# Performance work log

Hardware: AMD Instinct MI355X
Metric: run time of the kernel (lower is better)

## Reference

```python
import jax, jax.numpy as jnp
import numpy as np

B, T, C, H = 8, 2048, 1024, 64  # batch, time(block_size), n_embd, head_size


def setup_inputs() -> dict:
    key = jax.random.key(0)
    k1, k2, k3, k4 = jax.random.split(key, 4)
    x = jax.random.normal(k1, (B, T, C), dtype=jnp.float32)
    # nn.Linear(n_embd, head_size, bias=False): y = x @ W.T with W [H, C];
    # store as [C, H] so projection is x @ W.
    Wq = jax.random.normal(k2, (C, H), dtype=jnp.float32) * 0.02
    Wk = jax.random.normal(k3, (C, H), dtype=jnp.float32) * 0.02
    Wv = jax.random.normal(k4, (C, H), dtype=jnp.float32) * 0.02
    return {"x": x, "Wq": Wq, "Wk": Wk, "Wv": Wv}


def reference(x, Wq, Wk, Wv):
    # x: [B, T, C]
    Bb, Tt, Cc = x.shape
    q = x @ Wq  # [B, T, H]
    k = x @ Wk  # [B, T, H]
    v = x @ Wv  # [B, T, H]
    # scores = Q @ K^T / sqrt(channels)  -- note: code scales by n_embd, not head_size
    scale = jnp.asarray(Cc, x.dtype) ** 0.5
    scores = jnp.einsum('bth,bsh->bts', q, k) / scale  # [B, T, T]
    # causal mask (decoder=True): lower-triangular allowed
    causal = jnp.tril(jnp.ones((Tt, Tt), dtype=bool))
    scores = jnp.where(causal, scores, -jnp.inf)
    attn = jax.nn.softmax(scores, axis=-1)  # [B, T, T]
    # dropout p=0.0 -> identity
    res = attn @ v  # [B, T, H]
    return res, attn
```

## Files before the change

kernel.cpp:

```cpp
#include <hip/hip_runtime.h>
#include <hip/hip_bf16.h>


typedef __attribute__((ext_vector_type(8))) short bf16x8;
typedef __attribute__((ext_vector_type(4))) float f32x4;

#define NB 8
#define NT 2048
#define NC 1024
#define NH 64

#define VM_DRAIN() asm volatile("s_waitcnt vmcnt(0)" ::: "memory")

__device__ __forceinline__ unsigned short f2bf(float f) {
    unsigned int u = __builtin_bit_cast(unsigned int, f);
    u += 0x7fffu + ((u >> 16) & 1u);
    return (unsigned short)(u >> 16);
}

__device__ __forceinline__ bf16x8 cvt8(float4 a, float4 b) {
    union { bf16x8 v; __hip_bfloat162 h[4]; } u;
    u.h[0] = __float22bfloat162_rn(make_float2(a.x, a.y));
    u.h[1] = __float22bfloat162_rn(make_float2(a.z, a.w));
    u.h[2] = __float22bfloat162_rn(make_float2(b.x, b.y));
    u.h[3] = __float22bfloat162_rn(make_float2(b.z, b.w));
    return u.v;
}

__device__ __forceinline__ void async_ld16(const void* g, const void* l) {
    __builtin_amdgcn_global_load_lds(
        (const __attribute__((address_space(1))) unsigned int*)g,
        (__attribute__((address_space(3))) unsigned int*)(unsigned int)(unsigned long long)l,
        16, 0, 0);
}

__global__ __launch_bounds__(256) void wt_kernel(
        const float* __restrict__ Wq,
        const float* __restrict__ Wk,
        const float* __restrict__ Wv,
        unsigned short* __restrict__ Wt) {
    __shared__ float tile[64][65];
    int m  = blockIdx.x >> 4;
    int k0 = (blockIdx.x & 15) * 64;
    const float* W = (m == 0) ? Wq : ((m == 1) ? Wk : Wv);
    int tid = threadIdx.x;
    for (int i = 0; i < 4; ++i) {
        int f = tid + i * 256;
        int r = f >> 4, c4 = (f & 15) * 4;
        float4 v = *(const float4*)&W[(size_t)(k0 + r) * 64 + c4];
        tile[r][c4 + 0] = v.x; tile[r][c4 + 1] = v.y;
        tile[r][c4 + 2] = v.z; tile[r][c4 + 3] = v.w;
    }
    __syncthreads();
    int n  = tid & 63;
    int kq = (tid >> 6) * 16;
    float scale = (m == 0) ? 0.03125f : 1.0f;
    __attribute__((aligned(16))) unsigned short outv[16];
    for (int j = 0; j < 16; ++j)
        outv[j] = f2bf(tile[kq + j][n] * scale);
    unsigned short* dst = &Wt[(size_t)m * (64 * 1024) + (size_t)n * 1024 + k0 + kq];
    *(uint4*)dst       = *(const uint4*)&outv[0];
    *(uint4*)(dst + 8) = *(const uint4*)&outv[8];
}

__global__ __launch_bounds__(256) void qkv_kernel(
        const float* __restrict__ x,
        const unsigned short* __restrict__ Wt,
        unsigned short* __restrict__ qkv,
        unsigned short* __restrict__ v_t) {
    __shared__ char smem[65536];

    int tid  = threadIdx.x;
    int wave = tid >> 6, lane = tid & 63, quad = lane >> 4, l15 = lane & 15;
    int row0 = blockIdx.x * 32;

    f32x4 acc[2][3];
#pragma unroll
    for (int rt = 0; rt < 2; ++rt)
#pragma unroll
        for (int j = 0; j < 3; ++j) acc[rt][j] = (f32x4){0.f, 0.f, 0.f, 0.f};

#pragma unroll
    for (int i = 0; i < 2; ++i) {
        int s = i * 256 + tid;
        int m = s >> 4, p = s & 15;
        int j = (p & 8) | ((p & 7) ^ (m & 7));
        async_ld16(x + (size_t)(row0 + m) * NC + j * 4,
                   smem + i * 4096 + wave * 1024);
    }
#pragma unroll
    for (int i = 0; i < 6; ++i) {
        int s = i * 256 + tid;
        int n = s >> 3, p = s & 7;
        int j = p ^ (n & 7);
        async_ld16(Wt + (size_t)n * NC + j * 8,
                   smem + 8192 + i * 4096 + wave * 1024);
    }

    int cur = 0;
    for (int kb = 0; kb < 16; ++kb) {
        VM_DRAIN();
        __syncthreads();
        if (kb < 15) {
            char* nb = smem + (cur ^ 1) * 32768;
#pragma unroll
            for (int i = 0; i < 2; ++i) {
                int s = i * 256 + tid;
                int m = s >> 4, p = s & 15;
                int j = (p & 8) | ((p & 7) ^ (m & 7));
                async_ld16(x + (size_t)(row0 + m) * NC + (kb + 1) * 64 + j * 4,
                           nb + i * 4096 + wave * 1024);
            }
#pragma unroll
            for (int i = 0; i < 6; ++i) {
                int s = i * 256 + tid;
                int n = s >> 3, p = s & 7;
                int j = p ^ (n & 7);
                async_ld16(Wt + (size_t)n * NC + (kb + 1) * 64 + j * 8,
                           nb + 8192 + i * 4096 + wave * 1024);
            }
        }
        char* Ab = smem + cur * 32768;
        char* Bb = Ab + 8192;
#pragma unroll
        for (int c = 0; c < 2; ++c) {
            bf16x8 af[2];
#pragma unroll
            for (int rt = 0; rt < 2; ++rt) {
                int m  = rt * 16 + l15;
                int j0 = c * 8 + quad * 2;
                int p0 = (j0 & 8) | ((j0 & 7) ^ (m & 7));
                int p1 = (j0 & 8) | (((j0 + 1) & 7) ^ (m & 7));
                float4 a0 = *(const float4*)(Ab + m * 256 + p0 * 16);
                float4 a1 = *(const float4*)(Ab + m * 256 + p1 * 16);
                af[rt] = cvt8(a0, a1);
            }
#pragma unroll
            for (int jj = 0; jj < 3; ++jj) {
                int n = (wave * 3 + jj) * 16 + l15;
                int p = (c * 4 + quad) ^ (n & 7);
                bf16x8 bf = *(const bf16x8*)(Bb + n * 128 + p * 16);
#pragma unroll
                for (int rt = 0; rt < 2; ++rt)
                    acc[rt][jj] = __builtin_amdgcn_mfma_f32_16x16x32_bf16(
                        af[rt], bf, acc[rt][jj], 0, 0, 0);
            }
        }
        cur ^= 1;
    }

    int b = row0 >> 11;
#pragma unroll
    for (int jj = 0; jj < 3; ++jj) {
        int g   = wave * 3 + jj;
        int mat = g >> 2;
        int col = (g & 3) * 16 + l15;
#pragma unroll
        for (int rt = 0; rt < 2; ++rt) {
            int rowb = row0 + rt * 16 + quad * 4;
            if (mat < 2) {
#pragma unroll
                for (int r = 0; r < 4; ++r)
                    qkv[(size_t)mat * (16384 * 64) + (size_t)(rowb + r) * 64 + col] =
                        f2bf(acc[rt][jj][r]);
            } else {
                union { unsigned long long q; unsigned short us[4]; } pk;
#pragma unroll
                for (int r = 0; r < 4; ++r) pk.us[r] = f2bf(acc[rt][jj][r]);
                *(unsigned long long*)&v_t[((size_t)b * 64 + col) * NT + (rowb & 2047)] = pk.q;
            }
        }
    }
}

__global__ __launch_bounds__(256) void fattn_kernel(
        const unsigned short* __restrict__ qg,
        const unsigned short* __restrict__ kg,
        const unsigned short* __restrict__ vtg,
        float* __restrict__ res,
        float* __restrict__ attn) {
    __shared__ unsigned short kt[2 * 64 * 64];
    __shared__ unsigned short vt[2 * 64 * 64];
    __shared__ float ptf[32 * 68];
    __shared__ float rsred[2][32];
    __shared__ float rinv_s[32];
    char* ktb = (char*)kt;
    char* vtb = (char*)vt;

    int gx  = blockIdx.x;
    int b   = blockIdx.y;
    int rsp = gx & 1;
    int j   = gx >> 1;
    int it  = (b & 4) ? (31 - j) : j;
    int tid = threadIdx.x;
    int wave = tid >> 6, lane = tid & 63, quad = lane >> 4, l15 = lane & 15;
    int wr = wave & 1, wc = wave >> 1;
    int tb = it * 64 + rsp * 32;
    size_t brow = (size_t)b * NT;

    bf16x8 qf[2];
    {
        const unsigned short* qp = qg + (brow + tb + wr * 16 + l15) * NH + quad * 8;
        qf[0] = *(const bf16x8*)qp;
        qf[1] = *(const bf16x8*)(qp + 32);
    }
    int trow[4];
#pragma unroll
    for (int r = 0; r < 4; ++r) trow[r] = tb + wr * 16 + quad * 4 + r;

    float rs[4] = {0.f, 0.f, 0.f, 0.f};

#pragma unroll
    for (int i = 0; i < 2; ++i) {
        int s = i * 256 + tid;
        int r = s >> 3, p = s & 7;
        int jj = p ^ (r & 7);
        async_ld16(kg + (brow + r) * NH + jj * 8,
                   ktb + i * 4096 + wave * 1024);
    }
    int cur = 0;
    for (int st = 0; st <= it; ++st) {
        VM_DRAIN();
        __syncthreads();
        if (st + 1 <= it) {
#pragma unroll
            for (int i = 0; i < 2; ++i) {
                int s = i * 256 + tid;
                int r = s >> 3, p = s & 7;
                int jj = p ^ (r & 7);
                async_ld16(kg + (brow + (st + 1) * 64 + r) * NH + jj * 8,
                           ktb + (cur ^ 1) * 8192 + i * 4096 + wave * 1024);
            }
        }
        char* kb = ktb + cur * 8192;

        f32x4 sacc[2];
        sacc[0] = (f32x4){0.f, 0.f, 0.f, 0.f};
        sacc[1] = (f32x4){0.f, 0.f, 0.f, 0.f};
#pragma unroll
        for (int c = 0; c < 2; ++c)
#pragma unroll
            for (int ntl = 0; ntl < 2; ++ntl) {
                int n = wc * 32 + ntl * 16 + l15;
                int p = (c * 4 + quad) ^ (n & 7);
                bf16x8 kf = *(const bf16x8*)(kb + n * 128 + p * 16);
                sacc[ntl] = __builtin_amdgcn_mfma_f32_16x16x32_bf16(
                    qf[c], kf, sacc[ntl], 0, 0, 0);
            }
        bool dia = (st == it);
#pragma unroll
        for (int ntl = 0; ntl < 2; ++ntl) {
            int s_g = st * 64 + wc * 32 + ntl * 16 + l15;
#pragma unroll
            for (int r = 0; r < 4; ++r) {
                float e = __expf(sacc[ntl][r]);
                if (dia && s_g > trow[r]) e = 0.f;
                rs[r] += e;
            }
        }
        cur ^= 1;
    }

#pragma unroll
    for (int r = 0; r < 4; ++r) {
        float v = rs[r];
        v += __shfl_xor(v, 1, 16);
        v += __shfl_xor(v, 2, 16);
        v += __shfl_xor(v, 4, 16);
        v += __shfl_xor(v, 8, 16);
        if (l15 == 0) rsred[wc][wr * 16 + quad * 4 + r] = v;
    }
    __syncthreads();
    if (tid < 32) rinv_s[tid] = 1.0f / (rsred[0][tid] + rsred[1][tid]);
    __syncthreads();
    float rinv[4];
#pragma unroll
    for (int r = 0; r < 4; ++r) rinv[r] = rinv_s[wr * 16 + quad * 4 + r];

#pragma unroll
    for (int i = 0; i < 2; ++i) {
        int s = i * 256 + tid;
        int r = s >> 3, p = s & 7;
        int jj = p ^ (r & 7);
        async_ld16(kg + (brow + r) * NH + jj * 8,
                   ktb + i * 4096 + wave * 1024);
        async_ld16(vtg + ((size_t)b * 64 + r) * NT + jj * 8,
                   vtb + i * 4096 + wave * 1024);
    }
    cur = 0;
    f32x4 oacc[2];
    oacc[0] = (f32x4){0.f, 0.f, 0.f, 0.f};
    oacc[1] = (f32x4){0.f, 0.f, 0.f, 0.f};

    for (int st = 0; st <= it; ++st) {
        VM_DRAIN();
        __syncthreads();
        if (st + 1 <= it) {
#pragma unroll
            for (int i = 0; i < 2; ++i) {
                int s = i * 256 + tid;
                int r = s >> 3, p = s & 7;
                int jj = p ^ (r & 7);
                async_ld16(kg + (brow + (st + 1) * 64 + r) * NH + jj * 8,
                           ktb + (cur ^ 1) * 8192 + i * 4096 + wave * 1024);
                async_ld16(vtg + ((size_t)b * 64 + r) * NT + (st + 1) * 64 + jj * 8,
                           vtb + (cur ^ 1) * 8192 + i * 4096 + wave * 1024);
            }
        }
        char* kb = ktb + cur * 8192;
        char* vb = vtb + cur * 8192;

        f32x4 sacc[2];
        sacc[0] = (f32x4){0.f, 0.f, 0.f, 0.f};
        sacc[1] = (f32x4){0.f, 0.f, 0.f, 0.f};
#pragma unroll
        for (int c = 0; c < 2; ++c)
#pragma unroll
            for (int ntl = 0; ntl < 2; ++ntl) {
                int n = wc * 32 + ntl * 16 + l15;
                int p = (c * 4 + quad) ^ (n & 7);
                bf16x8 kf = *(const bf16x8*)(kb + n * 128 + p * 16);
                sacc[ntl] = __builtin_amdgcn_mfma_f32_16x16x32_bf16(
                    qf[c], kf, sacc[ntl], 0, 0, 0);
            }

        bool dia = (st == it);
#pragma unroll
        for (int ntl = 0; ntl < 2; ++ntl) {
            int s_g = st * 64 + wc * 32 + ntl * 16 + l15;
#pragma unroll
            for (int r = 0; r < 4; ++r) {
                float p = __expf(sacc[ntl][r]) * rinv[r];
                if (dia && s_g > trow[r]) p = 0.f;
                ptf[(wr * 16 + quad * 4 + r) * 68 + wc * 32 + ntl * 16 + l15] = p;
            }
        }
        __syncthreads();

#pragma unroll
        for (int k = 0; k < 2; ++k) {
            int f = k * 256 + tid;
            int row = f >> 4, c4 = (f & 15) * 4;
            *(float4*)&attn[(brow + tb + row) * NT + st * 64 + c4] =
                *(const float4*)&ptf[row * 68 + c4];
        }
        if (st < it) {
            float4 z4 = {0.f, 0.f, 0.f, 0.f};
#pragma unroll
            for (int k = 0; k < 2; ++k) {
                int f = k * 256 + tid;
                int row = f >> 4, c4 = (f & 15) * 4;
                *(float4*)&attn[(brow + st * 64 + rsp * 32 + row) * NT + it * 64 + c4] = z4;
            }
        }

#pragma unroll
        for (int c = 0; c < 2; ++c) {
            const float* pp = &ptf[(wr * 16 + l15) * 68 + c * 32 + quad * 8];
            float4 a0 = *(const float4*)pp;
            float4 a1 = *(const float4*)(pp + 4);
            bf16x8 pf = cvt8(a0, a1);
#pragma unroll
            for (int ntl = 0; ntl < 2; ++ntl) {
                int n = wc * 32 + ntl * 16 + l15;
                int p = (c * 4 + quad) ^ (n & 7);
                bf16x8 vf = *(const bf16x8*)(vb + n * 128 + p * 16);
                oacc[ntl] = __builtin_amdgcn_mfma_f32_16x16x32_bf16(
                    pf, vf, oacc[ntl], 0, 0, 0);
            }
        }
        cur ^= 1;
    }

#pragma unroll
    for (int ntl = 0; ntl < 2; ++ntl)
#pragma unroll
        for (int r = 0; r < 4; ++r)
            res[(size_t)(brow + trow[r]) * NH + wc * 32 + ntl * 16 + l15] = oacc[ntl][r];
}

extern "C" void kernel_launch(void* const* d_in, const int* in_sizes, int n_in,
                              void* d_out, int out_size, void* d_ws, size_t ws_size,
                              hipStream_t stream) {
    const float* x  = (const float*)d_in[0];
    const float* Wq = (const float*)d_in[1];
    const float* Wk = (const float*)d_in[2];
    const float* Wv = (const float*)d_in[3];

    unsigned short* ws  = (unsigned short*)d_ws;
    unsigned short* Wt  = ws;
    unsigned short* qkv = ws + 3 * 64 * 1024;
    unsigned short* v_t = qkv + 2 * 16384 * 64;

    float* res  = (float*)d_out;
    float* attn = res + (size_t)NB * NT * NH;

    hipLaunchKernelGGL(wt_kernel, dim3(48), dim3(256), 0, stream, Wq, Wk, Wv, Wt);
    hipLaunchKernelGGL(qkv_kernel, dim3(512), dim3(256), 0, stream, x, Wt, qkv, v_t);

    const unsigned short* qg = qkv;
    const unsigned short* kg = qkv + 16384 * 64;

    hipLaunchKernelGGL(fattn_kernel, dim3(64, 8), dim3(256), 0, stream,
                       qg, kg, v_t, res, attn);
}
```

Measured before the change: 220.1 us.

## Fuse weight transpose, QKV projection and attention into one persistent kernel

Merges the three kernels (weight transpose, QKV projection, causal attention) into a single 512-block kernel. Phases are separated by a software grid barrier built from atomic counters kept in workspace, and the counters are reset with a memset before each launch. The goal is to drop the launch overhead and idle gaps between kernels. In exchange it adds barrier spin cost. The barrier also depends on all 512 blocks being resident at once, since it uses a normal launch rather than a cooperative one, and the attention phase now runs with 64KB of static LDS, which may lower occupancy.

```diff
diff --git a/kernel.cpp b/kernel.cpp
--- a/kernel.cpp
+++ b/kernel.cpp
@@ -9,6 +9,7 @@
 #define NT 2048
 #define NC 1024
 #define NH 64
+#define NBLK 512
 
 #define VM_DRAIN() asm volatile("s_waitcnt vmcnt(0)" ::: "memory")
 
@@ -34,349 +35,371 @@
         16, 0, 0);
 }
 
-__global__ __launch_bounds__(256) void wt_kernel(
+__device__ __forceinline__ void grid_barrier(unsigned* cnt, unsigned* gen, int tid) {
+    __syncthreads();
+    if (tid == 0) {
+        __threadfence();
+        unsigned g = __hip_atomic_load(gen, __ATOMIC_ACQUIRE, __HIP_MEMORY_SCOPE_AGENT);
+        unsigned a = __hip_atomic_fetch_add(cnt, 1u, __ATOMIC_ACQ_REL, __HIP_MEMORY_SCOPE_AGENT);
+        if (a == NBLK - 1u) {
+            __hip_atomic_store(cnt, 0u, __ATOMIC_RELAXED, __HIP_MEMORY_SCOPE_AGENT);
+            __hip_atomic_fetch_add(gen, 1u, __ATOMIC_RELEASE, __HIP_MEMORY_SCOPE_AGENT);
+        } else {
+            while (__hip_atomic_load(gen, __ATOMIC_ACQUIRE, __HIP_MEMORY_SCOPE_AGENT) == g)
+                __builtin_amdgcn_s_sleep(2);
+        }
+        __threadfence();
+    }
+    __syncthreads();
+}
+
+__global__ __launch_bounds__(256) void mega_kernel(
+        const float* __restrict__ x,
         const float* __restrict__ Wq,
         const float* __restrict__ Wk,
         const float* __restrict__ Wv,
-        unsigned short* __restrict__ Wt) {
-    __shared__ float tile[64][65];
-    int m  = blockIdx.x >> 4;
-    int k0 = (blockIdx.x & 15) * 64;
-    const float* W = (m == 0) ? Wq : ((m == 1) ? Wk : Wv);
-    int tid = threadIdx.x;
-    for (int i = 0; i < 4; ++i) {
-        int f = tid + i * 256;
-        int r = f >> 4, c4 = (f & 15) * 4;
-        float4 v = *(const float4*)&W[(size_t)(k0 + r) * 64 + c4];
-        tile[r][c4 + 0] = v.x; tile[r][c4 + 1] = v.y;
-        tile[r][c4 + 2] = v.z; tile[r][c4 + 3] = v.w;
-    }
-    __syncthreads();
-    int n  = tid & 63;
-    int kq = (tid >> 6) * 16;
-    float scale = (m == 0) ? 0.03125f : 1.0f;
-    __attribute__((aligned(16))) unsigned short outv[16];
-    for (int j = 0; j < 16; ++j)
-        outv[j] = f2bf(tile[kq + j][n] * scale);
-    unsigned short* dst = &Wt[(size_t)m * (64 * 1024) + (size_t)n * 1024 + k0 + kq];
-    *(uint4*)dst       = *(const uint4*)&outv[0];
-    *(uint4*)(dst + 8) = *(const uint4*)&outv[8];
-}
-
-__global__ __launch_bounds__(256) void qkv_kernel(
-        const float* __restrict__ x,
-        const unsigned short* __restrict__ Wt,
+        unsigned short* __restrict__ Wt,
         unsigned short* __restrict__ qkv,
-        unsigned short* __restrict__ v_t) {
-    __shared__ char smem[65536];
-
+        unsigned short* __restrict__ v_t,
+        float* __restrict__ res,
+        float* __restrict__ attn,
+        unsigned* __restrict__ flags) {
+    __shared__ __align__(16) char smem[65536];
+
+    int bx   = blockIdx.x;
     int tid  = threadIdx.x;
     int wave = tid >> 6, lane = tid & 63, quad = lane >> 4, l15 = lane & 15;
-    int row0 = blockIdx.x * 32;
-
-    f32x4 acc[2][3];
-#pragma unroll
-    for (int rt = 0; rt < 2; ++rt)
-#pragma unroll
-        for (int j = 0; j < 3; ++j) acc[rt][j] = (f32x4){0.f, 0.f, 0.f, 0.f};
-
-#pragma unroll
-    for (int i = 0; i < 2; ++i) {
-        int s = i * 256 + tid;
-        int m = s >> 4, p = s & 15;
-        int j = (p & 8) | ((p & 7) ^ (m & 7));
-        async_ld16(x + (size_t)(row0 + m) * NC + j * 4,
-                   smem + i * 4096 + wave * 1024);
+    unsigned* cnt = flags;
+    unsigned* gen = flags + 1;
+
+    if (bx < 48) {
+        float* tile = (float*)smem;
+        int m  = bx >> 4;
+        int k0 = (bx & 15) * 64;
+        const float* W = (m == 0) ? Wq : ((m == 1) ? Wk : Wv);
+        for (int i = 0; i < 4; ++i) {
+            int f = tid + i * 256;
+            int r = f >> 4, c4 = (f & 15) * 4;
+            float4 v = *(const float4*)&W[(size_t)(k0 + r) * 64 + c4];
+            tile[r * 65 + c4 + 0] = v.x; tile[r * 65 + c4 + 1] = v.y;
+            tile[r * 65 + c4 + 2] = v.z; tile[r * 65 + c4 + 3] = v.w;
+        }
+        __syncthreads();
+        int n  = tid & 63;
+        int kq = (tid >> 6) * 16;
+        float scale = (m == 0) ? 0.03125f : 1.0f;
+        __attribute__((aligned(16))) unsigned short outv[16];
+        for (int j = 0; j < 16; ++j)
+            outv[j] = f2bf(tile[(kq + j) * 65 + n] * scale);
+        unsigned short* dst = &Wt[(size_t)m * (64 * 1024) + (size_t)n * 1024 + k0 + kq];
+        *(uint4*)dst       = *(const uint4*)&outv[0];
+        *(uint4*)(dst + 8) = *(const uint4*)&outv[8];
     }
-#pragma unroll
-    for (int i = 0; i < 6; ++i) {
-        int s = i * 256 + tid;
-        int n = s >> 3, p = s & 7;
-        int j = p ^ (n & 7);
-        async_ld16(Wt + (size_t)n * NC + j * 8,
-                   smem + 8192 + i * 4096 + wave * 1024);
+    grid_barrier(cnt, gen, tid);
+
+    {
+        int row0 = bx * 32;
+
+        f32x4 acc[2][3];
+#pragma unroll
+        for (int rt = 0; rt < 2; ++rt)
+#pragma unroll
+            for (int j = 0; j < 3; ++j) acc[rt][j] = (f32x4){0.f, 0.f, 0.f, 0.f};
+
+#pragma unroll
+        for (int i = 0; i < 2; ++i) {
+            int s = i * 256 + tid;
+            int m = s >> 4, p = s & 15;
+            int j = (p & 8) | ((p & 7) ^ (m & 7));
+            async_ld16(x + (size_t)(row0 + m) * NC + j * 4,
+                       smem + i * 4096 + wave * 1024);
+        }
+#pragma unroll
+        for (int i = 0; i < 6; ++i) {
+            int s = i * 256 + tid;
+            int n = s >> 3, p = s & 7;
+            int j = p ^ (n & 7);
+            async_ld16(Wt + (size_t)n * NC + j * 8,
+                       smem + 8192 + i * 4096 + wave * 1024);
+        }
+
+        int cur = 0;
+        for (int kb = 0; kb < 16; ++kb) {
+            VM_DRAIN();
+            __syncthreads();
+            if (kb < 15) {
+                char* nb = smem + (cur ^ 1) * 32768;
+#pragma unroll
+                for (int i = 0; i < 2; ++i) {
+                    int s = i * 256 + tid;
+                    int m = s >> 4, p = s & 15;
+                    int j = (p & 8) | ((p & 7) ^ (m & 7));
+                    async_ld16(x + (size_t)(row0 + m) * NC + (kb + 1) * 64 + j * 4,
+                               nb + i * 4096 + wave * 1024);
+                }
+#pragma unroll
+                for (int i = 0; i < 6; ++i) {
+                    int s = i * 256 + tid;
+                    int n = s >> 3, p = s & 7;
+                    int j = p ^ (n & 7);
+                    async_ld16(Wt + (size_t)n * NC + (kb + 1) * 64 + j * 8,
+                               nb + 8192 + i * 4096 + wave * 1024);
+                }
+            }
+            char* Ab = smem + cur * 32768;
+            char* Bb = Ab + 8192;
+#pragma unroll
+            for (int c = 0; c < 2; ++c) {
+                bf16x8 af[2];
+#pragma unroll
+                for (int rt = 0; rt < 2; ++rt) {
+                    int m  = rt * 16 + l15;
+                    int j0 = c * 8 + quad * 2;
+                    int p0 = (j0 & 8) | ((j0 & 7) ^ (m & 7));
+                    int p1 = (j0 & 8) | (((j0 + 1) & 7) ^ (m & 7));
+                    float4 a0 = *(const float4*)(Ab + m * 256 + p0 * 16);
+                    float4 a1 = *(const float4*)(Ab + m * 256 + p1 * 16);
+                    af[rt] = cvt8(a0, a1);
+                }
+#pragma unroll
+                for (int jj = 0; jj < 3; ++jj) {
+                    int n = (wave * 3 + jj) * 16 + l15;
+                    int p = (c * 4 + quad) ^ (n & 7);
+                    bf16x8 bf = *(const bf16x8*)(Bb + n * 128 + p * 16);
+#pragma unroll
+                    for (int rt = 0; rt < 2; ++rt)
+                        acc[rt][jj] = __builtin_amdgcn_mfma_f32_16x16x32_bf16(
+                            af[rt], bf, acc[rt][jj], 0, 0, 0);
+                }
+            }
+            cur ^= 1;
+        }
+
+        int b = row0 >> 11;
+#pragma unroll
+        for (int jj = 0; jj < 3; ++jj) {
+            int g   = wave * 3 + jj;
+            int mat = g >> 2;
+            int col = (g & 3) * 16 + l15;
+#pragma unroll
+            for (int rt = 0; rt < 2; ++rt) {
+                int rowb = row0 + rt * 16 + quad * 4;
+                if (mat < 2) {
+#pragma unroll
+                    for (int r = 0; r < 4; ++r)
+                        qkv[(size_t)mat * (16384 * 64) + (size_t)(rowb + r) * 64 + col] =
+                            f2bf(acc[rt][jj][r]);
+                } else {
+                    union { unsigned long long q; unsigned short us[4]; } pk;
+#pragma unroll
+                    for (int r = 0; r < 4; ++r) pk.us[r] = f2bf(acc[rt][jj][r]);
+                    *(unsigned long long*)&v_t[((size_t)b * 64 + col) * NT + (rowb & 2047)] = pk.q;
+                }
+            }
+        }
     }
-
-    int cur = 0;
-    for (int kb = 0; kb < 16; ++kb) {
-        VM_DRAIN();
+    grid_barrier(cnt, gen, tid);
+
+    {
+        const unsigned short* qg  = qkv;
+        const unsigned short* kg  = qkv + 16384 * 64;
+        const unsigned short* vtg = v_t;
+
+        char*  ktb    = smem;
+        char*  vtb    = smem + 16384;
+        float* ptf    = (float*)(smem + 32768);
+        float* rsred  = (float*)(smem + 41472);
+        float* rinv_s = (float*)(smem + 41728);
+
+        int gx  = bx & 63;
+        int b   = bx >> 6;
+        int rsp = gx & 1;
+        int j   = gx >> 1;
+        int it  = (b & 4) ? (31 - j) : j;
+        int wr = wave & 1, wc = wave >> 1;
+        int tb = it * 64 + rsp * 32;
+        size_t brow = (size_t)b * NT;
+
+        bf16x8 qf[2];
+        {
+            const unsigned short* qp = qg + (brow + tb + wr * 16 + l15) * NH + quad * 8;
+            qf[0] = *(const bf16x8*)qp;
+            qf[1] = *(const bf16x8*)(qp + 32);
+        }
+        int trow[4];
+#pragma unroll
+        for (int r = 0; r < 4; ++r) trow[r] = tb + wr * 16 + quad * 4 + r;
+
+        float rs[4] = {0.f, 0.f, 0.f, 0.f};
+
+#pragma unroll
+        for (int i = 0; i < 2; ++i) {
+            int s = i * 256 + tid;
+            int r = s >> 3, p = s & 7;
+            int jj = p ^ (r & 7);
+            async_ld16(kg + (brow + r) * NH + jj * 8,
+                       ktb + i * 4096 + wave * 1024);
+        }
+        int cur = 0;
+        for (int st = 0; st <= it; ++st) {
+            VM_DRAIN();
+            __syncthreads();
+            if (st + 1 <= it) {
+#pragma unroll
+                for (int i = 0; i < 2; ++i) {
+                    int s = i * 256 + tid;
+                    int r = s >> 3, p = s & 7;
+                    int jj = p ^ (r & 7);
+                    async_ld16(kg + (brow + (st + 1) * 64 + r) * NH + jj * 8,
+                               ktb + (cur ^ 1) * 8192 + i * 4096 + wave * 1024);
+                }
+            }
+            char* kb = ktb + cur * 8192;
+
+            f32x4 sacc[2];
+            sacc[0] = (f32x4){0.f, 0.f, 0.f, 0.f};
+            sacc[1] = (f32x4){0.f, 0.f, 0.f, 0.f};
+#pragma unroll
+            for (int c = 0; c < 2; ++c)
+#pragma unroll
+                for (int ntl = 0; ntl < 2; ++ntl) {
+                    int n = wc * 32 + ntl * 16 + l15;
+                    int p = (c * 4 + quad) ^ (n & 7);
+                    bf16x8 kf = *(const bf16x8*)(kb + n * 128 + p * 16);
+                    sacc[ntl] = __builtin_amdgcn_mfma_f32_16x16x32_bf16(
+                        qf[c], kf, sacc[ntl], 0, 0, 0);
+                }
+            bool dia = (st == it);
+#pragma unroll
+            for (int ntl = 0; ntl < 2; ++ntl) {
+                int s_g = st * 64 + wc * 32 + ntl * 16 + l15;
+#pragma unroll
+                for (int r = 0; r < 4; ++r) {
+                    float e = __expf(sacc[ntl][r]);
+                    if (dia && s_g > trow[r]) e = 0.f;
+                    rs[r] += e;
+                }
+            }
+            cur ^= 1;
+        }
+
+#pragma unroll
+        for (int r = 0; r < 4; ++r) {
+            float v = rs[r];
+            v += __shfl_xor(v, 1, 16);
+            v += __shfl_xor(v, 2, 16);
+            v += __shfl_xor(v, 4, 16);
+            v += __shfl_xor(v, 8, 16);
+            if (l15 == 0) rsred[wc * 32 + wr * 16 + quad * 4 + r] = v;
+        }
         __syncthreads();
-        if (kb < 15) {
-            char* nb = smem + (cur ^ 1) * 32768;
-#pragma unroll
-            for (int i = 0; i < 2; ++i) {
-                int s = i * 256 + tid;
-                int m = s >> 4, p = s & 15;
-                int j = (p & 8) | ((p & 7) ^ (m & 7));
-                async_ld16(x + (size_t)(row0 + m) * NC + (kb + 1) * 64 + j * 4,
-                           nb + i * 4096 + wave * 1024);
-            }
-#pragma unroll
-            for (int i = 0; i < 6; ++i) {
-                int s = i * 256 + tid;
-                int n = s >> 3, p = s & 7;
-                int j = p ^ (n & 7);
-                async_ld16(Wt + (size_t)n * NC + (kb + 1) * 64 + j * 8,
-                           nb + 8192 + i * 4096 + wave * 1024);
-            }
-        }
-        char* Ab = smem + cur * 32768;
-        char* Bb = Ab + 8192;
-#pragma unroll
-        for (int c = 0; c < 2; ++c) {
-            bf16x8 af[2];
-#pragma unroll
-            for (int rt = 0; rt < 2; ++rt) {
-                int m  = rt * 16 + l15;
-                int j0 = c * 8 + quad * 2;
-                int p0 = (j0 & 8) | ((j0 & 7) ^ (m & 7));
-                int p1 = (j0 & 8) | (((j0 + 1) & 7) ^ (m & 7));
-                float4 a0 = *(const float4*)(Ab + m * 256 + p0 * 16);
-                float4 a1 = *(const float4*)(Ab + m * 256 + p1 * 16);
-                af[rt] = cvt8(a0, a1);
-            }
-#pragma unroll
-            for (int jj = 0; jj < 3; ++jj) {
-                int n = (wave * 3 + jj) * 16 + l15;
-                int p = (c * 4 + quad) ^ (n & 7);
-                bf16x8 bf = *(const bf16x8*)(Bb + n * 128 + p * 16);
-#pragma unroll
-                for (int rt = 0; rt < 2; ++rt)
-                    acc[rt][jj] = __builtin_amdgcn_mfma_f32_16x16x32_bf16(
-                        af[rt], bf, acc[rt][jj], 0, 0, 0);
-            }
-        }
-        cur ^= 1;
-    }
-
-    int b = row0 >> 11;
-#pragma unroll
-    for (int jj = 0; jj < 3; ++jj) {
-        int g   = wave * 3 + jj;
-        int mat = g >> 2;
-        int col = (g & 3) * 16 + l15;
-#pragma unroll
-        for (int rt = 0; rt < 2; ++rt) {
-            int rowb = row0 + rt * 16 + quad * 4;
-            if (mat < 2) {
-#pragma unroll
-                for (int r = 0; r < 4; ++r)
-                    qkv[(size_t)mat * (16384 * 64) + (size_t)(rowb + r) * 64 + col] =
-                        f2bf(acc[rt][jj][r]);
-            } else {
-                union { unsigned long long q; unsigned short us[4]; } pk;
-#pragma unroll
-                for (int r = 0; r < 4; ++r) pk.us[r] = f2bf(acc[rt][jj][r]);
-                *(unsigned long long*)&v_t[((size_t)b * 64 + col) * NT + (rowb & 2047)] = pk.q;
-            }
-        }
-    }
-}
-
-__global__ __launch_bounds__(256) void fattn_kernel(
-        const unsigned short* __restrict__ qg,
-        const unsigned short* __restrict__ kg,
-        const unsigned short* __restrict__ vtg,
-        float* __restrict__ res,
-        float* __restrict__ attn) {
-    __shared__ unsigned short kt[2 * 64 * 64];
-    __shared__ unsigned short vt[2 * 64 * 64];
-    __shared__ float ptf[32 * 68];
-    __shared__ float rsred[2][32];
-    __shared__ float rinv_s[32];
-    char* ktb = (char*)kt;
-    char* vtb = (char*)vt;
-
-    int gx  = blockIdx.x;
-    int b   = blockIdx.y;
-    int rsp = gx & 1;
-    int j   = gx >> 1;
-    int it  = (b & 4) ? (31 - j) : j;
-    int tid = threadIdx.x;
-    int wave = tid >> 6, lane = tid & 63, quad = lane >> 4, l15 = lane & 15;
-    int wr = wave & 1, wc = wave >> 1;
-    int tb = it * 64 + rsp * 32;
-    size_t brow = (size_t)b * NT;
-
-    bf16x8 qf[2];
-    {
-        const unsigned short* qp = qg + (brow + tb + wr * 16 + l15) * NH + quad * 8;
-        qf[0] = *(const bf16x8*)qp;
-        qf[1] = *(const bf16x8*)(qp + 32);
-    }
-    int trow[4];
-#pragma unroll
-    for (int r = 0; r < 4; ++r) trow[r] = tb + wr * 16 + quad * 4 + r;
-
-    float rs[4] = {0.f, 0.f, 0.f, 0.f};
-
-#pragma unroll
-    for (int i = 0; i < 2; ++i) {
-        int s = i * 256 + tid;
-        int r = s >> 3, p = s & 7;
-        int jj = p ^ (r & 7);
-        async_ld16(kg + (brow + r) * NH + jj * 8,
-                   ktb + i * 4096 + wave * 1024);
-    }
-    int cur = 0;
-    for (int st = 0; st <= it; ++st) {
-        VM_DRAIN();
+        if (tid < 32) rinv_s[tid] = 1.0f / (rsred[tid] + rsred[32 + tid]);
         __syncthreads();
-        if (st + 1 <= it) {
-#pragma unroll
-            for (int i = 0; i < 2; ++i) {
-                int s = i * 256 + tid;
-                int r = s >> 3, p = s & 7;
-                int jj = p ^ (r & 7);
-                async_ld16(kg + (brow + (st + 1) * 64 + r) * NH + jj * 8,
-                           ktb + (cur ^ 1) * 8192 + i * 4096 + wave * 1024);
-            }
-        }
-        char* kb = ktb + cur * 8192;
-
-        f32x4 sacc[2];
-        sacc[0] = (f32x4){0.f, 0.f, 0.f, 0.f};
-        sacc[1] = (f32x4){0.f, 0.f, 0.f, 0.f};
-#pragma unroll
-        for (int c = 0; c < 2; ++c)
+        float rinv[4];
+#pragma unroll
+        for (int r = 0; r < 4; ++r) rinv[r] = rinv_s[wr * 16 + quad * 4 + r];
+
+#pragma unroll
+        for (int i = 0; i < 2; ++i) {
+            int s = i * 256 + tid;
+            int r = s >> 3, p = s & 7;
+            int jj = p ^ (r & 7);
+            async_ld16(kg + (brow + r) * NH + jj * 8,
+                       ktb + i * 4096 + wave * 1024);
+            async_ld16(vtg + ((size_t)b * 64 + r) * NT + jj * 8,
+                       vtb + i * 4096 + wave * 1024);
+        }
+        cur = 0;
+        f32x4 oacc[2];
+        oacc[0] = (f32x4){0.f, 0.f, 0.f, 0.f};
+        oacc[1] = (f32x4){0.f, 0.f, 0.f, 0.f};
+
+        for (int st = 0; st <= it; ++st) {
+            VM_DRAIN();
+            __syncthreads();
+            if (st + 1 <= it) {
+#pragma unroll
+                for (int i = 0; i < 2; ++i) {
+                    int s = i * 256 + tid;
+                    int r = s >> 3, p = s & 7;
+                    int jj = p ^ (r & 7);
+                    async_ld16(kg + (brow + (st + 1) * 64 + r) * NH + jj * 8,
+                               ktb + (cur ^ 1) * 8192 + i * 4096 + wave * 1024);
+                    async_ld16(vtg + ((size_t)b * 64 + r) * NT + (st + 1) * 64 + jj * 8,
+                               vtb + (cur ^ 1) * 8192 + i * 4096 + wave * 1024);
+                }
+            }
+            char* kb = ktb + cur * 8192;
+            char* vb = vtb + cur * 8192;
+
+            f32x4 sacc[2];
+            sacc[0] = (f32x4){0.f, 0.f, 0.f, 0.f};
+            sacc[1] = (f32x4){0.f, 0.f, 0.f, 0.f};
+#pragma unroll
+            for (int c = 0; c < 2; ++c)
+#pragma unroll
+                for (int ntl = 0; ntl < 2; ++ntl) {
+                    int n = wc * 32 + ntl * 16 + l15;
+                    int p = (c * 4 + quad) ^ (n & 7);
+                    bf16x8 kf = *(const bf16x8*)(kb + n * 128 + p * 16);
+                    sacc[ntl] = __builtin_amdgcn_mfma_f32_16x16x32_bf16(
+                        qf[c], kf, sacc[ntl], 0, 0, 0);
+                }
+
+            bool dia = (st == it);
 #pragma unroll
             for (int ntl = 0; ntl < 2; ++ntl) {
-                int n = wc * 32 + ntl * 16 + l15;
-                int p = (c * 4 + quad) ^ (n & 7);
-                bf16x8 kf = *(const bf16x8*)(kb + n * 128 + p * 16);
-                sacc[ntl] = __builtin_amdgcn_mfma_f32_16x16x32_bf16(
-                    qf[c], kf, sacc[ntl], 0, 0, 0);
-            }
-        bool dia = (st == it);
-#pragma unroll
-        for (int ntl = 0; ntl < 2; ++ntl) {
-            int s_g = st * 64 + wc * 32 + ntl * 16 + l15;
-#pragma unroll
-            for (int r = 0; r < 4; ++r) {
-                float e = __expf(sacc[ntl][r]);
-                if (dia && s_g > trow[r]) e = 0.f;
-                rs[r] += e;
-            }
-        }
-        cur ^= 1;
-    }
-
-#pragma unroll
-    for (int r = 0; r < 4; ++r) {
-        float v = rs[r];
-        v += __shfl_xor(v, 1, 16);
-        v += __shfl_xor(v, 2, 16);
-        v += __shfl_xor(v, 4, 16);
-        v += __shfl_xor(v, 8, 16);
-        if (l15 == 0) rsred[wc][wr * 16 + quad * 4 + r] = v;
-    }
-    __syncthreads();
-    if (tid < 32) rinv_s[tid] = 1.0f / (rsred[0][tid] + rsred[1][tid]);
-    __syncthreads();
-    float rinv[4];
-#pragma unroll
-    for (int r = 0; r < 4; ++r) rinv[r] = rinv_s[wr * 16 + quad * 4 + r];
-
-#pragma unroll
-    for (int i = 0; i < 2; ++i) {
-        int s = i * 256 + tid;
-        int r = s >> 3, p = s & 7;
-        int jj = p ^ (r & 7);
-        async_ld16(kg + (brow + r) * NH + jj * 8,
-                   ktb + i * 4096 + wave * 1024);
-        async_ld16(vtg + ((size_t)b * 64 + r) * NT + jj * 8,
-                   vtb + i * 4096 + wave * 1024);
-    }
-    cur = 0;
-    f32x4 oacc[2];
-    oacc[0] = (f32x4){0.f, 0.f, 0.f, 0.f};
-    oacc[1] = (f32x4){0.f, 0.f, 0.f, 0.f};
-
-    for (int st = 0; st <= it; ++st) {
-        VM_DRAIN();
-        __syncthreads();
-        if (st + 1 <= it) {
-#pragma unroll
-            for (int i = 0; i < 2; ++i) {
-                int s = i * 256 + tid;
-                int r = s >> 3, p = s & 7;
-                int jj = p ^ (r & 7);
-                async_ld16(kg + (brow + (st + 1) * 64 + r) * NH + jj * 8,
-                           ktb + (cur ^ 1) * 8192 + i * 4096 + wave * 1024);
-                async_ld16(vtg + ((size_t)b * 64 + r) * NT + (st + 1) * 64 + jj * 8,
-                           vtb + (cur ^ 1) * 8192 + i * 4096 + wave * 1024);
-            }
-        }
-        char* kb = ktb + cur * 8192;
-        char* vb = vtb + cur * 8192;
-
-        f32x4 sacc[2];
-        sacc[0] = (f32x4){0.f, 0.f, 0.f, 0.f};
-        sacc[1] = (f32x4){0.f, 0.f, 0.f, 0.f};
-#pragma unroll
-        for (int c = 0; c < 2; ++c)
-#pragma unroll
-            for (int ntl = 0; ntl < 2; ++ntl) {
-                int n = wc * 32 + ntl * 16 + l15;
-                int p = (c * 4 + quad) ^ (n & 7);
-                bf16x8 kf = *(const bf16x8*)(kb + n * 128 + p * 16);
-                sacc[ntl] = __builtin_amdgcn_mfma_f32_16x16x32_bf16(
-                    qf[c], kf, sacc[ntl], 0, 0, 0);
-            }
-
-        bool dia = (st == it);
-#pragma unroll
-        for (int ntl = 0; ntl < 2; ++ntl) {
-            int s_g = st * 64 + wc * 32 + ntl * 16 + l15;
-#pragma unroll
-            for (int r = 0; r < 4; ++r) {
-                float p = __expf(sacc[ntl][r]) * rinv[r];
-                if (dia && s_g > trow[r]) p = 0.f;
-                ptf[(wr * 16 + quad * 4 + r) * 68 + wc * 32 + ntl * 16 + l15] = p;
-            }
-        }
-        __syncthreads();
-
-#pragma unroll
-        for (int k = 0; k < 2; ++k) {
-            int f = k * 256 + tid;
-            int row = f >> 4, c4 = (f & 15) * 4;
-            *(float4*)&attn[(brow + tb + row) * NT + st * 64 + c4] =
-                *(const float4*)&ptf[row * 68 + c4];
-        }
-        if (st < it) {
-            float4 z4 = {0.f, 0.f, 0.f, 0.f};
+                int s_g = st * 64 + wc * 32 + ntl * 16 + l15;
+#pragma unroll
+                for (int r = 0; r < 4; ++r) {
+                    float p = __expf(sacc[ntl][r]) * rinv[r];
+                    if (dia && s_g > trow[r]) p = 0.f;
+                    ptf[(wr * 16 + quad * 4 + r) * 68 + wc * 32 + ntl * 16 + l15] = p;
+                }
+            }
+            __syncthreads();
+
 #pragma unroll
             for (int k = 0; k < 2; ++k) {
                 int f = k * 256 + tid;
                 int row = f >> 4, c4 = (f & 15) * 4;
-                *(float4*)&attn[(brow + st * 64 + rsp * 32 + row) * NT + it * 64 + c4] = z4;
-            }
-        }
-
-#pragma unroll
-        for (int c = 0; c < 2; ++c) {
-            const float* pp = &ptf[(wr * 16 + l15) * 68 + c * 32 + quad * 8];
-            float4 a0 = *(const float4*)pp;
-            float4 a1 = *(const float4*)(pp + 4);
-            bf16x8 pf = cvt8(a0, a1);
-#pragma unroll
-            for (int ntl = 0; ntl < 2; ++ntl) {
-                int n = wc * 32 + ntl * 16 + l15;
-                int p = (c * 4 + quad) ^ (n & 7);
-                bf16x8 vf = *(const bf16x8*)(vb + n * 128 + p * 16);
-                oacc[ntl] = __builtin_amdgcn_mfma_f32_16x16x32_bf16(
-                    pf, vf, oacc[ntl], 0, 0, 0);
-            }
-        }
-        cur ^= 1;
+                *(float4*)&attn[(brow + tb + row) * NT + st * 64 + c4] =
+                    *(const float4*)&ptf[row * 68 + c4];
+            }
+            if (st < it) {
+                float4 z4 = {0.f, 0.f, 0.f, 0.f};
+#pragma unroll
+                for (int k = 0; k < 2; ++k) {
+                    int f = k * 256 + tid;
+                    int row = f >> 4, c4 = (f & 15) * 4;
+                    *(float4*)&attn[(brow + st * 64 + rsp * 32 + row) * NT + it * 64 + c4] = z4;
+                }
+            }
+
+#pragma unroll
+            for (int c = 0; c < 2; ++c) {
+                const float* pp = &ptf[(wr * 16 + l15) * 68 + c * 32 + quad * 8];
+                float4 a0 = *(const float4*)pp;
+                float4 a1 = *(const float4*)(pp + 4);
+                bf16x8 pf = cvt8(a0, a1);
+#pragma unroll
+                for (int ntl = 0; ntl < 2; ++ntl) {
+                    int n = wc * 32 + ntl * 16 + l15;
+                    int p = (c * 4 + quad) ^ (n & 7);
+                    bf16x8 vf = *(const bf16x8*)(vb + n * 128 + p * 16);
+                    oacc[ntl] = __builtin_amdgcn_mfma_f32_16x16x32_bf16(
+                        pf, vf, oacc[ntl], 0, 0, 0);
+                }
+            }
+            cur ^= 1;
+        }
+
+#pragma unroll
+        for (int ntl = 0; ntl < 2; ++ntl)
+#pragma unroll
+            for (int r = 0; r < 4; ++r)
+                res[(size_t)(brow + trow[r]) * NH + wc * 32 + ntl * 16 + l15] = oacc[ntl][r];
     }
-
-#pragma unroll
-    for (int ntl = 0; ntl < 2; ++ntl)
-#pragma unroll
-        for (int r = 0; r < 4; ++r)
-            res[(size_t)(brow + trow[r]) * NH + wc * 32 + ntl * 16 + l15] = oacc[ntl][r];
 }
 
 extern "C" void kernel_launch(void* const* d_in, const int* in_sizes, int n_in,
@@ -391,16 +414,17 @@
     unsigned short* Wt  = ws;
     unsigned short* qkv = ws + 3 * 64 * 1024;
     unsigned short* v_t = qkv + 2 * 16384 * 64;
+    unsigned* flags = (unsigned*)(v_t + 16384 * 64);
 
     float* res  = (float*)d_out;
     float* attn = res + (size_t)NB * NT * NH;
 
-    hipLaunchKernelGGL(wt_kernel, dim3(48), dim3(256), 0, stream, Wq, Wk, Wv, Wt);
-    hipLaunchKernelGGL(qkv_kernel, dim3(512), dim3(256), 0, stream, x, Wt, qkv, v_t);
-
-    const unsigned short* qg = qkv;
-    const unsigned short* kg = qkv + 16384 * 64;
-
-    hipLaunchKernelGGL(fattn_kernel, dim3(64, 8), dim3(256), 0, stream,
-                       qg, kg, v_t, res, attn);
-}
+    hipMemsetAsync(flags, 0, 2 * sizeof(unsigned), stream);
+
+    void* kargs[] = {(void*)&x, (void*)&Wq, (void*)&Wk, (void*)&Wv, (void*)&Wt,
+                     (void*)&qkv, (void*)&v_t, (void*)&res, (void*)&attn,
+                     (void*)&flags};
+    hipLaunchKernelGGL(mega_kernel, dim3(NBLK), dim3(256), 0, stream,
+                       x, Wq, Wk, Wv, Wt, qkv, v_t, res, attn, flags);
+    (void)kargs;
+}
```

Result: slower. 386.7 us (+75.7%).
